# Performance work log

Hardware: AMD Instinct MI355X
Metric: run time of the kernel (lower is better)

The kernel has to match this reference:

```python
import jax, jax.numpy as jnp
import numpy as np

B, C, X, Y, Z = 2, 4, 128, 128, 96
_BIG = 1e10  # effectively infinite squared distance (no background in line)


def _edt_sq_pass(f, axis):
    """One separable pass of the exact squared EDT along `axis`:
    g[i] = min_j f[j] + (i - j)^2  (Felzenszwalb lower envelope, brute-forced
    with lax.map so only O(rest) memory per step)."""
    f = jnp.moveaxis(f, axis, -1)  # (..., L)
    idx = jnp.arange(f.shape[-1], dtype=f.dtype)
    g = jax.lax.map(lambda i: jnp.min(f + (i - idx) ** 2, axis=-1), idx)  # (L, ...)
    return jnp.moveaxis(jnp.moveaxis(g, 0, -1), -1, axis)


def _edt(mask):
    """Exact Euclidean distance of True voxels to the nearest False voxel
    (matches scipy.ndimage.distance_transform_edt on a binary mask)."""
    f = jnp.where(mask, _BIG, 0.0).astype(jnp.float32)
    for ax in (-3, -2, -1):  # three spatial axes
        f = _edt_sq_pass(f, ax)
    return jnp.sqrt(f)


def _neighbor(m, axis, d):
    """Shift `m` by d along `axis` with edge replication (reflect border,
    as in skimage's grey erosion used by find_boundaries)."""
    axis = axis % m.ndim
    pw = [(1, 1) if i == axis else (0, 0) for i in range(m.ndim)]
    p = jnp.pad(m, pw, mode='edge')
    sl = [slice(None)] * m.ndim
    sl[axis] = slice(1 + d, p.shape[axis] - 1 + d)
    return p[tuple(sl)]


def _inner_boundary(m):
    """skimage find_boundaries(mode='inner', connectivity=1): foreground voxels
    with at least one background face-neighbor."""
    eroded = m
    for ax in (-3, -2, -1):
        eroded = eroded & _neighbor(m, ax, 1) & _neighbor(m, ax, -1)
    return m & ~eroded


def _compute_sdf(onehot):
    """Signed distance map per (batch, class): negdis - posdis, zero on the
    inner boundary; zero where the class is absent; channel 0 is skipped."""
    posdis = _edt(onehot)          # dist inside object to background
    negdis = _edt(~onehot)         # dist outside object to foreground
    sdf = jnp.where(_inner_boundary(onehot), 0.0, negdis - posdis)
    any_pos = jnp.any(onehot, axis=(2, 3, 4), keepdims=True)
    sdf = jnp.where(any_pos, sdf, 0.0)
    return sdf.at[:, 0].set(0.0)   # loop starts at c=1 in the original


def setup_inputs() -> dict:
    key = jax.random.key(0)
    k1, k2 = jax.random.split(key)
    net_output = jax.random.normal(k1, (B, C, X, Y, Z), dtype=jnp.float32)
    gt = jax.random.randint(k2, (B, 1, X, Y, Z), 0, C, dtype=jnp.int32)
    return {"net_output": net_output, "gt": gt}


def reference(net_output, gt):
    probs = jax.nn.softmax(net_output, axis=1)  # softmax_helper = softmax over class dim
    classes = jnp.arange(net_output.shape[1], dtype=gt.dtype).reshape(1, -1, 1, 1, 1)
    onehot = gt == classes  # scatter_(1, gt, 1) one-hot, bool (B,C,X,Y,Z)
    phi = _compute_sdf(onehot)
    # einsum('bcxyz,bcxyz->bcxyz') on foreground channels, then global mean
    return jnp.mean(probs[:, 1:] * phi[:, 1:])
```

## Files before the change

### kernel.cpp

```cpp
#include <hip/hip_runtime.h>
#include <hip/hip_fp16.h>
#include <math.h>

#define XD 128
#define YD 128
#define ZD 96
#define NV (XD*YD*ZD)
#define SXX (YD*ZD)
#define SENT 49152
#define TW2 114
#define TDW (TW2/2)
#define TROWS 144
#define SCANB 192
#define PROBB 1024

__global__ __launch_bounds__(384) void k_scan_prob(const int* __restrict__ gt,
                                                   const float* __restrict__ net,
                                                   unsigned char* __restrict__ out,
                                                   __half2* __restrict__ probs,
                                                   int* __restrict__ flags,
                                                   int batch0) {
    const int bb  = blockIdx.y;
    const int myb = batch0 + bb;
    const int tid = threadIdx.x;

    if (blockIdx.x >= SCANB) {
        const int p = (blockIdx.x - SCANB) * 384 + tid;
        const int idx = p * 4;
        const float* nb = net + (size_t)myb * 4 * NV;
        float4 v0 = *(const float4*)(nb + idx);
        float4 v1 = *(const float4*)(nb + NV + idx);
        float4 v2 = *(const float4*)(nb + 2 * NV + idx);
        float4 v3 = *(const float4*)(nb + 3 * NV + idx);

        const float a0[4] = {v0.x, v0.y, v0.z, v0.w};
        const float a1[4] = {v1.x, v1.y, v1.z, v1.w};
        const float a2[4] = {v2.x, v2.y, v2.z, v2.w};
        const float a3[4] = {v3.x, v3.y, v3.z, v3.w};
        float p1[4], p2[4], p3[4];
#pragma unroll
        for (int j = 0; j < 4; ++j) {
            float mx = fmaxf(fmaxf(a0[j], a1[j]), fmaxf(a2[j], a3[j]));
            float e0 = __expf(a0[j] - mx);
            float e1 = __expf(a1[j] - mx);
            float e2 = __expf(a2[j] - mx);
            float e3 = __expf(a3[j] - mx);
            float iv = __frcp_rn(e0 + e1 + e2 + e3);
            p1[j] = e1 * iv; p2[j] = e2 * iv; p3[j] = e3 * iv;
        }
        __half2 h10 = __floats2half2_rn(p1[0], p1[1]);
        __half2 h11 = __floats2half2_rn(p1[2], p1[3]);
        __half2 h20 = __floats2half2_rn(p2[0], p2[1]);
        __half2 h21 = __floats2half2_rn(p2[2], p2[3]);
        __half2 h30 = __floats2half2_rn(p3[0], p3[1]);
        __half2 h31 = __floats2half2_rn(p3[2], p3[3]);
        ((__half2*)probs)[(size_t)(myb * 3 + 0) * (NV / 2) + 2 * p]     = h10;
        ((__half2*)probs)[(size_t)(myb * 3 + 0) * (NV / 2) + 2 * p + 1] = h11;
        ((__half2*)probs)[(size_t)(myb * 3 + 1) * (NV / 2) + 2 * p]     = h20;
        ((__half2*)probs)[(size_t)(myb * 3 + 1) * (NV / 2) + 2 * p + 1] = h21;
        ((__half2*)probs)[(size_t)(myb * 3 + 2) * (NV / 2) + 2 * p]     = h30;
        ((__half2*)probs)[(size_t)(myb * 3 + 2) * (NV / 2) + 2 * p + 1] = h31;
        return;
    }

    const int l   = tid & 63;
    const int w6  = tid >> 6;
    const int lq0 = blockIdx.x * 64;

    __shared__ unsigned char gtile[64 * 132];
    __shared__ int blkbits;
    if (tid == 0) blkbits = 0;

    int mybits = 0;
    const int* gp = gt + (size_t)myb * NV + lq0 + l;
    for (int j = w6; j < XD; j += 6) {
        int g = gp[(size_t)j * SXX];
        mybits |= 1 << g;
        gtile[l * 132 + j] = (unsigned char)g;
    }
#pragma unroll
    for (int off = 32; off; off >>= 1) mybits |= __shfl_xor(mybits, off);
    __syncthreads();
    if ((tid & 63) == 0) atomicOr(&blkbits, mybits);

    unsigned int D[32];
    {
        const unsigned int ci = (unsigned int)((w6 >> 1) + 1);
        const int s = w6 & 1;
        unsigned int G[32];
        const unsigned int* grow = (const unsigned int*)gtile + l * 33;
#pragma unroll
        for (int q = 0; q < 32; ++q) G[q] = grow[q];

        int cnt = 200;
#pragma unroll
        for (int q = 0; q < 32; ++q) {
            unsigned int u = G[q], dv = 0;
#pragma unroll
            for (int b = 0; b < 4; ++b) {
                unsigned int gv = (u >> (8 * b)) & 255u;
                bool zero = s ? (gv == ci) : (gv != ci);
                cnt = zero ? 0 : ((cnt < 200) ? cnt + 1 : 200);
                dv |= (unsigned int)cnt << (8 * b);
            }
            D[q] = dv;
        }
        cnt = 200;
#pragma unroll
        for (int q = 31; q >= 0; --q) {
            unsigned int u = G[q], dv = D[q];
#pragma unroll
            for (int b = 3; b >= 0; --b) {
                unsigned int gv = (u >> (8 * b)) & 255u;
                bool zero = s ? (gv == ci) : (gv != ci);
                cnt = zero ? 0 : ((cnt < 200) ? cnt + 1 : 200);
                unsigned int old = (dv >> (8 * b)) & 255u;
                unsigned int nbv = ((unsigned int)cnt < old) ? (unsigned int)cnt : old;
                dv = (dv & ~(255u << (8 * b))) | (nbv << (8 * b));
            }
            D[q] = dv;
        }
    }
    __syncthreads();
    if (tid == 0) atomicOr(&flags[myb], blkbits);

    {
        const int r = l & 3;
        unsigned char* ob = out + (size_t)(bb * 6 + w6) * NV + lq0 + (l & ~3);
#pragma unroll
        for (int q = 0; q < 32; ++q) {
            unsigned int A = D[q];
            unsigned int Bv = (unsigned int)__shfl_xor((int)A, 1);
            unsigned int t = (r & 1)
                ? __builtin_amdgcn_perm(A, Bv, 0x07030501u)
                : __builtin_amdgcn_perm(A, Bv, 0x02060004u);
            unsigned int Cv = (unsigned int)__shfl_xor((int)t, 2);
            unsigned int y = (r & 2)
                ? __builtin_amdgcn_perm(t, Cv, 0x07060302u)
                : __builtin_amdgcn_perm(t, Cv, 0x01000504u);
            *(unsigned int*)(ob + (size_t)(4 * q + r) * SXX) = y;
        }
    }
}

__device__ __forceinline__ bool edt_fast(const float r[32], float m[16]) {
#pragma unroll
    for (int k = 0; k < 16; ++k) m[k] = r[k + 8];
#pragma unroll
    for (int t = 1; t <= 4; ++t) {
        const float t2 = (float)(t * t);
#pragma unroll
        for (int k = 0; k < 16; ++k)
            m[k] = fminf(m[k], fminf(r[k + 8 - t], r[k + 8 + t]) + t2);
    }
    float mm = m[0];
#pragma unroll
    for (int k = 1; k < 16; ++k) mm = fmaxf(mm, m[k]);
    if (__all(mm <= 16.0f)) return true;
#pragma unroll
    for (int t = 5; t <= 8; ++t) {
        const float t2 = (float)(t * t);
#pragma unroll
        for (int k = 0; k < 16; ++k)
            m[k] = fminf(m[k], fminf(r[k + 8 - t], r[k + 8 + t]) + t2);
    }
    mm = m[0];
#pragma unroll
    for (int k = 1; k < 16; ++k) mm = fmaxf(mm, m[k]);
    return __all(mm <= 64.0f) != 0;
}

template<int STRIDE, int L>
__device__ __forceinline__ void edt_slow(const unsigned short* __restrict__ p0,
                                         int i0, float m[16]) {
    int t = 9;
    bool done = false;
    while (!done && t < L) {
        for (int u = 0; u < 4; ++u, ++t) {
            float t2 = (float)(t * t);
#pragma unroll
            for (int k = 0; k < 16; ++k) {
                int jm = i0 + k - t; if (jm < -8) jm = -8;
                int jp = i0 + k + t; if (jp > L + 7) jp = L + 7;
                m[k] = fminf(m[k], fminf((float)p0[jm * STRIDE],
                                         (float)p0[jp * STRIDE]) + t2);
            }
        }
        float mm = m[0];
#pragma unroll
        for (int k = 1; k < 16; ++k) mm = fmaxf(mm, m[k]);
        done = __all(mm <= (float)((t - 1) * (t - 1))) != 0;
    }
}

__global__ __launch_bounds__(768) void k_pass_yz(const unsigned char* __restrict__ in,
                                                 unsigned short* __restrict__ zbuf,
                                                 const int* __restrict__ flags,
                                                 int batch0) {
    const int lv  = blockIdx.y;
    const int x   = blockIdx.x;
    const int tid = threadIdx.x;
    const int bbp = lv / 6;
    const int cp  = (lv % 6) >> 1;
    if (((flags[batch0 + bbp] >> (cp + 1)) & 1) == 0) return;

    __shared__ unsigned short tile[TROWS * TW2];
    unsigned int* t32 = (unsigned int*)tile;

    for (int i = tid; i < 16 * TDW; i += 768) {
        int r = i / TDW, c = i - r * TDW;
        int row = (r < 8) ? r : 128 + r;
        t32[row * TDW + c] = 0xFFFFFFFFu;
    }
    for (int i = tid; i < 128 * 9; i += 768) {
        int r = i / 9, c = i - r * 9;
        int col = (c < 4) ? c : (48 + c);
        t32[(8 + r) * TDW + col] = 0xFFFFFFFFu;
    }
    {
        const uint4* ip = (const uint4*)(in + (size_t)lv * NV + (size_t)x * SXX);
        uint4 v = ip[tid];
        int e = tid * 16;
        int y = e / ZD, z = e - y * ZD;
        unsigned int base = (8 + y) * TDW + (8 + z) / 2;
        unsigned int vv[4] = {v.x, v.y, v.z, v.w};
#pragma unroll
        for (int q = 0; q < 4; ++q) {
            unsigned int b0 = vv[q] & 255u, b1 = (vv[q] >> 8) & 255u;
            unsigned int b2 = (vv[q] >> 16) & 255u, b3 = vv[q] >> 24;
            t32[base + 2 * q] = (b0 > 127u ? SENT : b0 * b0) |
                                ((b1 > 127u ? SENT : b1 * b1) << 16);
            t32[base + 2 * q + 1] = (b2 > 127u ? SENT : b2 * b2) |
                                    ((b3 > 127u ? SENT : b3 * b3) << 16);
        }
    }
    __syncthreads();

    float m[16];
    {
        const int z0 = tid % 96;
        const int i0 = (tid / 96) * 16;
        float r[32];
#pragma unroll
        for (int w = 0; w < 32; ++w) r[w] = (float)tile[(i0 + w) * TW2 + 8 + z0];
        if (!edt_fast(r, m)) edt_slow<TW2, YD>(&tile[8 * TW2 + 8 + z0], i0, m);
        __syncthreads();
#pragma unroll
        for (int k = 0; k < 16; ++k)
            tile[(8 + i0 + k) * TW2 + 8 + z0] =
                (unsigned short)fminf(m[k], (float)SENT);
        __syncthreads();
    }
    {
        const int y0 = tid % 128;
        const int i0 = (tid / 128) * 16;
        float r[32];
        const unsigned int* wp = &t32[(8 + y0) * TDW + i0 / 2];
#pragma unroll
        for (int q = 0; q < 16; ++q) {
            unsigned int u = wp[q];
            r[2 * q] = (float)(u & 0xFFFFu);
            r[2 * q + 1] = (float)(u >> 16);
        }
        if (!edt_fast(r, m)) edt_slow<1, ZD>(&tile[(8 + y0) * TW2 + 8], i0, m);
        unsigned int* op = (unsigned int*)(zbuf + (size_t)lv * NV +
                                           (size_t)x * SXX +
                                           (size_t)y0 * ZD + i0);
#pragma unroll
        for (int q = 0; q < 8; ++q) {
            unsigned int u0 = (unsigned int)fminf(m[2 * q],     (float)SENT);
            unsigned int u1 = (unsigned int)fminf(m[2 * q + 1], (float)SENT);
            op[q] = u0 | (u1 << 16);
        }
    }
}

__global__ __launch_bounds__(256) void k_accum(const unsigned short* __restrict__ vols,
                                               const __half2* __restrict__ probs,
                                               const int* __restrict__ flags,
                                               double* __restrict__ partials,
                                               int batch0) {
    const int b = batch0 + blockIdx.y;
    const unsigned short* vb = vols + (size_t)blockIdx.y * 6 * NV;
    const int fbits = flags[b];
    double ls = 0.0;
    for (int p = blockIdx.x * 256 + threadIdx.x; p < NV / 2; p += 1024 * 256) {
        const int idx = p * 2;
        float acc = 0.0f;
#pragma unroll
        for (int ci = 1; ci <= 3; ++ci) {
            if ((fbits >> ci) & 1) {
                ushort2 dp = *(const ushort2*)(vb + (size_t)(2 * ci - 2) * NV + idx);
                ushort2 dn = *(const ushort2*)(vb + (size_t)(2 * ci - 1) * NV + idx);
                float2 pf = __half22float2(
                    probs[(size_t)(b * 3 + ci - 1) * (NV / 2) + p]);
                float phi0 = (dp.x == 1) ? 0.0f
                           : (sqrtf((float)dn.x) - sqrtf((float)dp.x));
                float phi1 = (dp.y == 1) ? 0.0f
                           : (sqrtf((float)dn.y) - sqrtf((float)dp.y));
                acc += pf.x * phi0 + pf.y * phi1;
            }
        }
        ls += (double)acc;
    }
    __shared__ double sd[256];
    sd[threadIdx.x] = ls;
    __syncthreads();
    for (int off = 128; off > 0; off >>= 1) {
        if (threadIdx.x < off) sd[threadIdx.x] += sd[threadIdx.x + off];
        __syncthreads();
    }
    if (threadIdx.x == 0) partials[(size_t)b * 1024 + blockIdx.x] = sd[0];
}

__global__ void k_reduce(const double* __restrict__ partials, int n,
                         float* __restrict__ out) {
    __shared__ double sd[256];
    double ls = 0.0;
    for (int i = threadIdx.x; i < n; i += 256) ls += partials[i];
    sd[threadIdx.x] = ls;
    __syncthreads();
    for (int off = 128; off > 0; off >>= 1) {
        if (threadIdx.x < off) sd[threadIdx.x] += sd[threadIdx.x + off];
        __syncthreads();
    }
    if (threadIdx.x == 0) out[0] = (float)(sd[0] / 9437184.0);
}

extern "C" void kernel_launch(void* const* d_in, const int* in_sizes, int n_in,
                              void* d_out, int out_size, void* d_ws, size_t ws_size,
                              hipStream_t stream) {
    const float* net = (const float*)d_in[0];
    const int*   gt  = (const int*)d_in[1];
    float* out = (float*)d_out;
    char* ws = (char*)d_ws;

    const size_t xbufB1 = (size_t)6 * NV;
    const size_t zbufB1 = (size_t)6 * NV * sizeof(unsigned short);
    const size_t probsB = (size_t)2 * 3 * NV * 2;
    const size_t tail   = (size_t)2048 * sizeof(double) + 64;

    const int nb = (ws_size >= 2 * (xbufB1 + zbufB1) + probsB + tail) ? 2 : 1;

    unsigned char*  xbuf = (unsigned char*)ws;
    unsigned short* zbuf = (unsigned short*)(ws + (size_t)nb * xbufB1);
    __half2*       probs = (__half2*)(ws + (size_t)nb * (xbufB1 + zbufB1));
    double*     partials = (double*)((char*)probs + probsB);
    int*           flags = (int*)((char*)partials + 2048 * sizeof(double));

    hipMemsetAsync(flags, 0, 8 * sizeof(int), stream);

    for (int b0 = 0; b0 < 2; b0 += nb) {
        hipLaunchKernelGGL(k_scan_prob, dim3(SCANB + PROBB, nb), dim3(384), 0,
                           stream, gt, net, xbuf, probs, flags, b0);
        hipLaunchKernelGGL(k_pass_yz, dim3(XD, 6 * nb), dim3(768), 0, stream,
                           xbuf, zbuf, flags, b0);
        hipLaunchKernelGGL(k_accum, dim3(1024, nb), dim3(256), 0, stream,
                           zbuf, probs, flags, partials, b0);
    }
    hipLaunchKernelGGL(k_reduce, dim3(1), dim3(256), 0, stream, partials,
                       2048, out);
}
```

Before: 84.06 us.

## Fuse YZ EDT pass with probability dot-product reduction, drop zbuf

```diff
diff --git a/kernel.cpp b/kernel.cpp
--- a/kernel.cpp
+++ b/kernel.cpp
@@ -193,28 +193,38 @@
     }
 }
 
-__global__ __launch_bounds__(768) void k_pass_yz(const unsigned char* __restrict__ in,
-                                                 unsigned short* __restrict__ zbuf,
+__global__ __launch_bounds__(768) void k_edt_dot(const unsigned char* __restrict__ in,
+                                                 const __half2* __restrict__ probs,
                                                  const int* __restrict__ flags,
+                                                 double* __restrict__ partials,
                                                  int batch0) {
-    const int lv  = blockIdx.y;
-    const int x   = blockIdx.x;
-    const int tid = threadIdx.x;
-    const int bbp = lv / 6;
-    const int cp  = (lv % 6) >> 1;
-    if (((flags[batch0 + bbp] >> (cp + 1)) & 1) == 0) return;
+    const int x    = blockIdx.x;
+    const int lv   = blockIdx.y;
+    const int bbl  = lv / 6;
+    const int slot = lv % 6;
+    const int c    = slot >> 1;
+    const int s    = slot & 1;
+    const int b    = batch0 + bbl;
+    const int tid  = threadIdx.x;
+    const int pidx = (b * 6 + slot) * XD + x;
 
     __shared__ unsigned short tile[TROWS * TW2];
+    __shared__ double sd[768];
     unsigned int* t32 = (unsigned int*)tile;
 
+    if (((flags[b] >> (c + 1)) & 1) == 0) {
+        if (tid == 0) partials[pidx] = 0.0;
+        return;
+    }
+
     for (int i = tid; i < 16 * TDW; i += 768) {
-        int r = i / TDW, c = i - r * TDW;
+        int r = i / TDW, cc = i - r * TDW;
         int row = (r < 8) ? r : 128 + r;
-        t32[row * TDW + c] = 0xFFFFFFFFu;
+        t32[row * TDW + cc] = 0xFFFFFFFFu;
     }
     for (int i = tid; i < 128 * 9; i += 768) {
-        int r = i / 9, c = i - r * 9;
-        int col = (c < 4) ? c : (48 + c);
+        int r = i / 9, cc = i - r * 9;
+        int col = (cc < 4) ? cc : (48 + cc);
         t32[(8 + r) * TDW + col] = 0xFFFFFFFFu;
     }
     {
@@ -251,9 +261,9 @@
                 (unsigned short)fminf(m[k], (float)SENT);
         __syncthreads();
     }
-    {
-        const int y0 = tid % 128;
-        const int i0 = (tid / 128) * 16;
+    const int y0 = tid % 128;
+    const int i0 = (tid / 128) * 16;
+    {
         float r[32];
         const unsigned int* wp = &t32[(8 + y0) * TDW + i0 / 2];
 #pragma unroll
@@ -263,54 +273,39 @@
             r[2 * q + 1] = (float)(u >> 16);
         }
         if (!edt_fast(r, m)) edt_slow<1, ZD>(&tile[(8 + y0) * TW2 + 8], i0, m);
-        unsigned int* op = (unsigned int*)(zbuf + (size_t)lv * NV +
-                                           (size_t)x * SXX +
-                                           (size_t)y0 * ZD + i0);
-#pragma unroll
-        for (int q = 0; q < 8; ++q) {
-            unsigned int u0 = (unsigned int)fminf(m[2 * q],     (float)SENT);
-            unsigned int u1 = (unsigned int)fminf(m[2 * q + 1], (float)SENT);
-            op[q] = u0 | (u1 << 16);
-        }
-    }
-}
-
-__global__ __launch_bounds__(256) void k_accum(const unsigned short* __restrict__ vols,
-                                               const __half2* __restrict__ probs,
-                                               const int* __restrict__ flags,
-                                               double* __restrict__ partials,
-                                               int batch0) {
-    const int b = batch0 + blockIdx.y;
-    const unsigned short* vb = vols + (size_t)blockIdx.y * 6 * NV;
-    const int fbits = flags[b];
-    double ls = 0.0;
-    for (int p = blockIdx.x * 256 + threadIdx.x; p < NV / 2; p += 1024 * 256) {
-        const int idx = p * 2;
-        float acc = 0.0f;
-#pragma unroll
-        for (int ci = 1; ci <= 3; ++ci) {
-            if ((fbits >> ci) & 1) {
-                ushort2 dp = *(const ushort2*)(vb + (size_t)(2 * ci - 2) * NV + idx);
-                ushort2 dn = *(const ushort2*)(vb + (size_t)(2 * ci - 1) * NV + idx);
-                float2 pf = __half22float2(
-                    probs[(size_t)(b * 3 + ci - 1) * (NV / 2) + p]);
-                float phi0 = (dp.x == 1) ? 0.0f
-                           : (sqrtf((float)dn.x) - sqrtf((float)dp.x));
-                float phi1 = (dp.y == 1) ? 0.0f
-                           : (sqrtf((float)dn.y) - sqrtf((float)dp.y));
-                acc += pf.x * phi0 + pf.y * phi1;
-            }
-        }
-        ls += (double)acc;
-    }
-    __shared__ double sd[256];
-    sd[threadIdx.x] = ls;
-    __syncthreads();
-    for (int off = 128; off > 0; off >>= 1) {
-        if (threadIdx.x < off) sd[threadIdx.x] += sd[threadIdx.x + off];
+    }
+
+    float a = 0.0f;
+    {
+        const __half2* pv = probs + (size_t)(b * 3 + c) * (NV / 2) +
+                            ((size_t)x * SXX + (size_t)y0 * ZD + i0) / 2;
+        if (s == 0) {
+#pragma unroll
+            for (int q = 0; q < 8; ++q) {
+                float2 pf = __half22float2(pv[q]);
+                float d0 = fminf(m[2 * q],     (float)SENT);
+                float d1 = fminf(m[2 * q + 1], (float)SENT);
+                float t0 = ((d0 == 1.0f) ? 1.0f : 0.0f) - sqrtf(d0);
+                float t1 = ((d1 == 1.0f) ? 1.0f : 0.0f) - sqrtf(d1);
+                a += pf.x * t0 + pf.y * t1;
+            }
+        } else {
+#pragma unroll
+            for (int q = 0; q < 8; ++q) {
+                float2 pf = __half22float2(pv[q]);
+                float d0 = fminf(m[2 * q],     (float)SENT);
+                float d1 = fminf(m[2 * q + 1], (float)SENT);
+                a += pf.x * sqrtf(d0) + pf.y * sqrtf(d1);
+            }
+        }
+    }
+    sd[tid] = (double)a;
+    __syncthreads();
+    for (int off = 512; off; off >>= 1) {
+        if (tid < off && tid + off < 768) sd[tid] += sd[tid + off];
         __syncthreads();
     }
-    if (threadIdx.x == 0) partials[(size_t)b * 1024 + blockIdx.x] = sd[0];
+    if (tid == 0) partials[pidx] = sd[0];
 }
 
 __global__ void k_reduce(const double* __restrict__ partials, int n,
@@ -336,28 +331,24 @@
     char* ws = (char*)d_ws;
 
     const size_t xbufB1 = (size_t)6 * NV;
-    const size_t zbufB1 = (size_t)6 * NV * sizeof(unsigned short);
     const size_t probsB = (size_t)2 * 3 * NV * 2;
-    const size_t tail   = (size_t)2048 * sizeof(double) + 64;
-
-    const int nb = (ws_size >= 2 * (xbufB1 + zbufB1) + probsB + tail) ? 2 : 1;
-
-    unsigned char*  xbuf = (unsigned char*)ws;
-    unsigned short* zbuf = (unsigned short*)(ws + (size_t)nb * xbufB1);
-    __half2*       probs = (__half2*)(ws + (size_t)nb * (xbufB1 + zbufB1));
+    const size_t tail   = (size_t)1536 * sizeof(double) + 64;
+
+    const int nb = (ws_size >= 2 * xbufB1 + probsB + tail) ? 2 : 1;
+
+    unsigned char* xbuf  = (unsigned char*)ws;
+    __half2*       probs = (__half2*)(ws + (size_t)nb * xbufB1);
     double*     partials = (double*)((char*)probs + probsB);
-    int*           flags = (int*)((char*)partials + 2048 * sizeof(double));
+    int*           flags = (int*)((char*)partials + 1536 * sizeof(double));
 
     hipMemsetAsync(flags, 0, 8 * sizeof(int), stream);
 
     for (int b0 = 0; b0 < 2; b0 += nb) {
         hipLaunchKernelGGL(k_scan_prob, dim3(SCANB + PROBB, nb), dim3(384), 0,
                            stream, gt, net, xbuf, probs, flags, b0);
-        hipLaunchKernelGGL(k_pass_yz, dim3(XD, 6 * nb), dim3(768), 0, stream,
-                           xbuf, zbuf, flags, b0);
-        hipLaunchKernelGGL(k_accum, dim3(1024, nb), dim3(256), 0, stream,
-                           zbuf, probs, flags, partials, b0);
+        hipLaunchKernelGGL(k_edt_dot, dim3(XD, 6 * nb), dim3(768), 0, stream,
+                           xbuf, probs, flags, partials, b0);
     }
     hipLaunchKernelGGL(k_reduce, dim3(1), dim3(256), 0, stream, partials,
-                       2048, out);
-}
+                       1536, out);
+}
```

New measurement: 79.68 us. 5.2% less time.
